# Kernel optimization log

Hardware: AMD Instinct MI355X
Metric: run time of the kernel (lower is better)

Reference implementation:

```python
import jax, jax.numpy as jnp
import numpy as np

N = 50000
E = 400000
C_IN = 32
H = 64
RATIO = 0.5
SEQ_LEN = 5


def setup_inputs() -> dict:
    key = jax.random.key(0)
    ks = jax.random.split(key, 12)
    x = jax.random.normal(ks[0], (N, C_IN), jnp.float32)
    row = jax.random.randint(ks[1], (E,), 0, N, jnp.int32)
    off = jax.random.randint(ks[2], (E,), 1, N, jnp.int32)
    col = ((row + off) % N).astype(jnp.int32)  # no self-loops
    edge_index = jnp.stack([row, col])
    mask = jax.random.uniform(ks[3], (N,)) < 0.5

    def g(k, shape, fan):
        return jax.random.normal(k, shape, jnp.float32) / np.float32(np.sqrt(fan))

    return {
        "x": x, "edge_index": edge_index, "mask": mask,
        "conv0_w": g(ks[4], (C_IN, H), C_IN), "conv0_b": jnp.zeros((H,), jnp.float32),
        "conv1_w": g(ks[5], (H, H), H), "conv1_b": jnp.zeros((H,), jnp.float32),
        "pool_w": g(ks[6], (H,), H),
        "up_w": g(ks[7], (H, H), H), "up_b": jnp.zeros((H,), jnp.float32),
        "lstm0_w_ih": g(ks[8], (4 * H, H), H), "lstm0_w_hh": g(ks[9], (4 * H, H), H),
        "lstm0_b_ih": jnp.zeros((4 * H,), jnp.float32), "lstm0_b_hh": jnp.zeros((4 * H,), jnp.float32),
        "fin_w_ih": g(ks[10], (4 * H, H), H), "fin_w_hh": g(ks[11], (4 * H, H), H),
        "fin_b_ih": jnp.zeros((4 * H,), jnp.float32), "fin_b_hh": jnp.zeros((4 * H,), jnp.float32),
    }


def _coalesce(row, col, w, n):
    # sum duplicate (row, col) entries; output sorted by (row, col)
    key = row.astype(np.int64) * n + col.astype(np.int64)
    uk, inv = np.unique(key, return_inverse=True)
    w2 = np.bincount(inv, weights=w.astype(np.float64), minlength=uk.shape[0]).astype(np.float32)
    return uk // n, uk % n, w2


def _augment_adj(row, col, w, n):
    # remove self loops, add self loops (weight 1), compute A @ A (sparse), remove self loops
    m = row != col
    row = np.concatenate([row[m].astype(np.int64), np.arange(n, dtype=np.int64)])
    col = np.concatenate([col[m].astype(np.int64), np.arange(n, dtype=np.int64)])
    w = np.concatenate([w[m].astype(np.float32), np.ones(n, np.float32)])
    row, col, w = _coalesce(row, col, w, n)  # CSR-ordered
    cnt = np.bincount(row, minlength=n)
    indptr = np.concatenate([[0], np.cumsum(cnt)])
    dk = cnt[col]                      # out-degree of middle node k for each edge (i,k)
    starts = indptr[col]
    total = int(dk.sum())
    seg = np.repeat(np.cumsum(dk) - dk, dk)
    gi = np.repeat(starts, dk) + (np.arange(total) - seg)
    oi = np.repeat(row, dk)
    oj = col[gi]
    ow = np.repeat(w, dk) * w[gi]
    r2, c2, w2 = _coalesce(oi, oj, ow, n)
    m2 = r2 != c2
    return r2[m2], c2[m2], w2[m2]


def _gcn(x, row, col, ew, n, W, b):
    # GCNConv(improved=True): self-loop weight 2.0, symmetric deg^-1/2 normalization,
    # aggregate messages at target (col)
    h = x @ W
    loop = jnp.arange(n, dtype=row.dtype)
    r = jnp.concatenate([row, loop])
    c = jnp.concatenate([col, loop])
    w = jnp.concatenate([ew, jnp.full((n,), 2.0, ew.dtype)])
    deg = jax.ops.segment_sum(w, c, num_segments=n)
    dinv = jnp.where(deg > 0, jax.lax.rsqrt(deg), 0.0)
    norm = dinv[r] * w * dinv[c]
    out = jax.ops.segment_sum(norm[:, None] * h[r], c, num_segments=n)
    return out + b


def _sequences(x, mi):
    # sliding window [idx-L+1, idx] per masked node, zero left-padded
    t = mi[:, None] + jnp.arange(SEQ_LEN)[None, :] - (SEQ_LEN - 1)  # [M, L]
    return jnp.where((t >= 0)[:, :, None], x[jnp.clip(t, 0)], 0.0)


def _lstm_last(seq, w_ih, w_hh, b_ih, b_hh):
    # torch LSTM gate order: i, f, g, o; zero init state; return last hidden
    h = jnp.zeros((seq.shape[0], w_hh.shape[1]), seq.dtype)
    c = jnp.zeros_like(h)
    def step(carry, xt):
        h, c = carry
        g = xt @ w_ih.T + h @ w_hh.T + b_ih + b_hh
        i, f, gg, o = jnp.split(g, 4, axis=-1)
        c = jax.nn.sigmoid(f) * c + jax.nn.sigmoid(i) * jnp.tanh(gg)
        h = jax.nn.sigmoid(o) * jnp.tanh(c)
        return (h, c), None
    (h, _), _ = jax.lax.scan(step, (h, c), jnp.swapaxes(seq, 0, 1))
    return h


def reference(x, edge_index, mask, conv0_w, conv0_b, conv1_w, conv1_b, pool_w,
              up_w, up_b, lstm0_w_ih, lstm0_w_hh, lstm0_b_ih, lstm0_b_hh,
              fin_w_ih, fin_w_hh, fin_b_ih, fin_b_hh):
    n = x.shape[0]
    row0, col0 = edge_index[0], edge_index[1]
    ew0 = jnp.ones((row0.shape[0],), x.dtype)

    # down conv 0
    x1 = jax.nn.relu(_gcn(x, row0, col0, ew0, n, conv0_w, conv0_b))

    # augment_adj: sparse (A+I)^2 without diagonal (structural, constant)
    r2, c2, w2 = _augment_adj(np.asarray(row0), np.asarray(col0),
                              np.ones(row0.shape[0], np.float32), n)

    # TopKPooling: score = tanh((x.w)/||w||), keep top ceil(ratio*n)
    score = jnp.tanh((x1 @ pool_w) / jnp.linalg.norm(pool_w))
    k = int(np.ceil(RATIO * n))
    perm = np.argsort(-np.asarray(score), kind="stable")[:k]
    remap = np.full(n, -1, np.int64)
    remap[perm] = np.arange(k)
    keep = (remap[r2] >= 0) & (remap[c2] >= 0)
    pr = jnp.asarray(remap[r2[keep]].astype(np.int32))
    pc = jnp.asarray(remap[c2[keep]].astype(np.int32))
    pw = jnp.asarray(w2[keep])
    permj = jnp.asarray(perm.astype(np.int32))
    xp = x1[permj] * score[permj][:, None]

    # down conv 1 on pooled graph
    x2 = jax.nn.relu(_gcn(xp, pr, pc, pw, k, conv1_w, conv1_b))

    # up path (depth=1): LSTM over skip features at masked nodes
    mi = jnp.asarray(np.where(np.asarray(mask))[0].astype(np.int32))
    h0 = _lstm_last(_sequences(x1, mi), lstm0_w_ih, lstm0_w_hh, lstm0_b_ih, lstm0_b_hh)
    res = x1.at[mi].set(h0)
    up = jnp.zeros_like(x1).at[permj].set(x2)
    xo = _gcn(res + up, row0, col0, ew0, n, up_w, up_b)  # last level: no activation

    # final LSTM on masked nodes
    hf = _lstm_last(_sequences(xo, mi), fin_w_ih, fin_w_hh, fin_b_ih, fin_b_hh)
    return xo.at[mi].set(hf)
```

## Files before the change

kernel.cpp:

```cpp
#include <hip/hip_runtime.h>
#include <math.h>

#define NN 50000
#define EE 400000
#define CINV 32
#define KKEEP 25000
#define SEQL 5
#define HASH_BITS 20
#define HASH_SIZE (1u<<HASH_BITS)
#define HASH_MASK (HASH_SIZE-1u)
#define HEMPTY 0xFFFFFFFFu
#define PSB 196

typedef float vf4 __attribute__((ext_vector_type(4)));

__device__ __forceinline__ float sigm(float x){ return __builtin_amdgcn_rcpf(1.f+__expf(-x)); }
__device__ __forceinline__ float ftanh(float x){ return 1.f - 2.f*__builtin_amdgcn_rcpf(1.f+__expf(2.f*x)); }

__global__ void k_init(uint2* __restrict__ hash, unsigned* __restrict__ hist,
                       int* __restrict__ degcnt, int* __restrict__ diagint,
                       int* __restrict__ fillc, int* __restrict__ minv,
                       unsigned* scal, unsigned long long* selp,
                       const float* __restrict__ w0, const float* __restrict__ b0i,
                       const float* __restrict__ b0h, const float* __restrict__ wf,
                       const float* __restrict__ bfi, const float* __restrict__ bfh,
                       float* __restrict__ WT0, float* __restrict__ WTf,
                       float* __restrict__ bs0, float* __restrict__ bsf){
  int i = blockIdx.x*256 + threadIdx.x;
  if (i < (int)HASH_SIZE) hash[i] = make_uint2(HEMPTY, 0u);
  if (i < 4*65536) hist[i] = 0u;
  if (i < NN){ degcnt[i]=0; diagint[i]=0; fillc[i]=0; minv[i]=-1; }
  if (i < 256*64){
    int r = i>>6, k = i&63;
    int dst = k*256 + (r&63)*4 + (r>>6);
    WT0[dst] = w0[i];
    WTf[dst] = wf[i];
  }
  if (i < 256){
    int dst = (i&63)*4 + (i>>6);
    bs0[dst]=b0i[i]+b0h[i]; bsf[dst]=bfi[i]+bfh[i];
  }
  if (i == 0){ scal[0]=0u; scal[1]=0u; scal[3]=KKEEP; selp[0]=0ull; }
}

__global__ void k_phase2(const int* __restrict__ row, const int* __restrict__ col,
                         const int* __restrict__ mp, int* __restrict__ degcnt,
                         uint2* __restrict__ tab, unsigned* scal,
                         const float* __restrict__ X, const float* __restrict__ W,
                         float* __restrict__ Y){
  int idx = blockIdx.x*256 + threadIdx.x;
  if (idx < EE){
    int c = col[idx];
    atomicAdd(&degcnt[c], 1);
    unsigned key = (unsigned)row[idx]*50000u + (unsigned)c;
    unsigned h = (key*2654435761u) >> (32-HASH_BITS);
    for(;;){
      unsigned old = atomicCAS(&tab[h].x, HEMPTY, key);
      if (old==HEMPTY || old==key){ atomicAdd(&tab[h].y, 1u); break; }
      h = (h+1)&HASH_MASK;
    }
  }
  if (idx < NN/4){ if ((unsigned)mp[idx] > 1u) atomicOr(&scal[1], 1u); }
  if (idx < NN*16){
    int i = idx>>4, fq = idx&15;
    const vf4* X4 = (const vf4*)&X[i*CINV];
    const vf4* W4 = (const vf4*)W;
    vf4 acc = {0.f,0.f,0.f,0.f};
    #pragma unroll
    for (int kq=0;kq<CINV/4;kq++){
      vf4 xv = X4[kq];
      #pragma unroll
      for (int u=0;u<4;u++) acc += xv[u] * W4[(kq*4+u)*16+fq];
    }
    ((vf4*)Y)[i*16+fq] = acc;
  }
}

__global__ void k_psum1(const int* __restrict__ deg, int* __restrict__ part,
                        int* __restrict__ bsum, float* __restrict__ dinv){
  __shared__ int sc[256];
  int b = blockIdx.x, t = threadIdx.x, i = b*256+t;
  int v = (i<NN) ? deg[i] : 0;
  if (i < NN) dinv[i] = rsqrtf((float)v + 2.0f);
  sc[t] = v; __syncthreads();
  for (int o=1;o<256;o<<=1){
    int x = (t>=o) ? sc[t-o] : 0;
    __syncthreads();
    sc[t] += x;
    __syncthreads();
  }
  if (i < NN) part[i] = sc[t]-v;
  if (t == 255) bsum[b] = sc[255];
}
__global__ void k_psum3(const int* __restrict__ part, const int* __restrict__ bsum,
                        int* __restrict__ indptr){
  __shared__ int sc[256];
  int t = threadIdx.x;
  int v = (t<PSB) ? bsum[t] : 0;
  sc[t] = v; __syncthreads();
  for (int o=1;o<256;o<<=1){
    int x = (t>=o) ? sc[t-o] : 0;
    __syncthreads();
    sc[t] += x;
    __syncthreads();
  }
  int bb = blockIdx.x;
  int ex = sc[bb] - ((bb<PSB) ? bsum[bb] : 0);
  int i = bb*256 + t;
  if (i < NN) indptr[i] = part[i] + ex;
  if (i == 0) indptr[NN] = EE;
}

__global__ void k_phase4(const int* __restrict__ row, const int* __restrict__ col,
                         const int* __restrict__ indptr, int* __restrict__ fillc,
                         int* __restrict__ csr_r, const uint2* __restrict__ tab,
                         int* __restrict__ diagint, const void* __restrict__ mp,
                         unsigned* scal, int* __restrict__ mlist, int* __restrict__ minv){
  int idx = blockIdx.x*256 + threadIdx.x;
  if (idx < EE){
    int r = row[idx], c = col[idx];
    int pos = indptr[c] + atomicAdd(&fillc[c], 1);
    csr_r[pos] = r;
    unsigned rkey = (unsigned)c*50000u + (unsigned)r;
    unsigned h = (rkey*2654435761u) >> (32-HASH_BITS);
    for(;;){
      unsigned kk = tab[h].x;
      if (kk==rkey){ atomicAdd(&diagint[r], (int)tab[h].y); break; }
      if (kk==HEMPTY) break;
      h = (h+1)&HASH_MASK;
    }
  } else {
    int i = idx - EE;
    if (i < NN){
      int mv = scal[1] ? (int)((const unsigned char*)mp)[i] : ((const int*)mp)[i];
      if (mv){ int p = (int)atomicAdd(&scal[0], 1u); mlist[p] = i; minv[i] = p; }
    }
  }
}

__global__ void k_mm64v(const float* __restrict__ X, const float* __restrict__ W, float* __restrict__ Y){
  int idx = blockIdx.x*256 + threadIdx.x;
  if (idx >= NN*16) return;
  int i = idx>>4, fq = idx&15;
  const vf4* X4 = (const vf4*)&X[i*64];
  const vf4* W4 = (const vf4*)W;
  vf4 acc = {0.f,0.f,0.f,0.f};
  #pragma unroll
  for (int kq=0;kq<16;kq++){
    vf4 xv = X4[kq];
    #pragma unroll
    for (int u=0;u<4;u++) acc += xv[u] * W4[(kq*4+u)*16+fq];
  }
  ((vf4*)Y)[i*16+fq] = acc;
}

__global__ void g_gcn0(const int* __restrict__ indptr, const int* __restrict__ csr_r,
                       const float* __restrict__ dinv, const float* __restrict__ H,
                       const float* __restrict__ b, const float* __restrict__ pw,
                       float* __restrict__ out, unsigned long long* __restrict__ keys,
                       float* __restrict__ score, unsigned* __restrict__ hist){
  int node = blockIdx.x*4 + (threadIdx.x>>6), lane = threadIdx.x&63;
  if (node >= NN) return;
  int s = __builtin_amdgcn_readfirstlane(indptr[node]);
  int e = __builtin_amdgcn_readfirstlane(indptr[node+1]);
  int deg = e - s;
  float a0=0.f,a1=0.f,a2=0.f,a3=0.f;
  for (int base=0; base<deg; base+=64){
    int take = min(64, deg-base);
    bool act = lane < take;
    int ii = act ? csr_r[s+base+lane] : 0;
    float dv = act ? dinv[ii] : 0.f;
    int j=0;
    for (; j+4<=take; j+=4){
      int r0=__shfl(ii,j,64), r1=__shfl(ii,j+1,64), r2=__shfl(ii,j+2,64), r3=__shfl(ii,j+3,64);
      float d0=__shfl(dv,j,64), d1=__shfl(dv,j+1,64), d2=__shfl(dv,j+2,64), d3=__shfl(dv,j+3,64);
      a0 += d0*H[(size_t)r0*64+lane];
      a1 += d1*H[(size_t)r1*64+lane];
      a2 += d2*H[(size_t)r2*64+lane];
      a3 += d3*H[(size_t)r3*64+lane];
    }
    for (; j<take; j++){
      int r0=__shfl(ii,j,64); float d0=__shfl(dv,j,64);
      a0 += d0*H[(size_t)r0*64+lane];
    }
  }
  float acc = (a0+a1)+(a2+a3);
  float di = dinv[node];
  float v = di*acc + 2.f*di*di*H[(size_t)node*64+lane] + b[lane];
  float x1v = fmaxf(v, 0.f);
  out[(size_t)node*64+lane] = x1v;
  float pv = pw[lane];
  float nq = pv*pv;
  float dq = x1v*pv;
  for (int o=32;o;o>>=1){ nq += __shfl_down(nq, o, 64); dq += __shfl_down(dq, o, 64); }
  if (lane==0){
    float sv = tanhf(dq / sqrtf(nq));
    sv = sv + 0.0f;
    score[node] = sv;
    unsigned u = __float_as_uint(sv);
    unsigned asc = (u>>31) ? ~u : (u | 0x80000000u);
    unsigned desc = ~asc;
    keys[node] = (((unsigned long long)desc)<<32) | (unsigned)node;
    atomicAdd(&hist[desc>>16], 1u);
  }
}
__global__ void g_t2(const int* __restrict__ indptr, const int* __restrict__ csr_r,
                     const float* __restrict__ dinv1, const float* __restrict__ hp,
                     float* __restrict__ t2){
  int node = blockIdx.x*4 + (threadIdx.x>>6), lane = threadIdx.x&63;
  if (node >= NN) return;
  int s = __builtin_amdgcn_readfirstlane(indptr[node]);
  int e = __builtin_amdgcn_readfirstlane(indptr[node+1]);
  int deg = e - s;
  float a0 = dinv1[node]*hp[(size_t)node*64+lane];
  float a1 = 0.f;
  for (int base=0; base<deg; base+=64){
    int take = min(64, deg-base);
    bool act = lane < take;
    int ii = act ? csr_r[s+base+lane] : 0;
    float dv = act ? dinv1[ii] : 0.f;
    int j=0;
    for (; j+2<=take; j+=2){
      float d0=__shfl(dv,j,64), d1=__shfl(dv,j+1,64);
      int r0=__shfl(ii,j,64), r1=__shfl(ii,j+1,64);
      if (d0!=0.f) a0 += d0*hp[(size_t)r0*64+lane];
      if (d1!=0.f) a1 += d1*hp[(size_t)r1*64+lane];
    }
    for (; j<take; j++){
      float d0=__shfl(dv,j,64); int r0=__shfl(ii,j,64);
      if (d0!=0.f) a0 += d0*hp[(size_t)r0*64+lane];
    }
  }
  t2[(size_t)node*64+lane] = a0+a1;
}
__global__ void g_agg2y(const int* __restrict__ indptr, const int* __restrict__ csr_r,
                        const float* __restrict__ t2, const float* __restrict__ hp,
                        const float* __restrict__ dinv1, const int* __restrict__ diagint,
                        const int* __restrict__ kp, const float* __restrict__ b1,
                        const float* __restrict__ C, const float* __restrict__ Hbuf,
                        const int* __restrict__ minv, float* __restrict__ D){
  int node = blockIdx.x*4 + (threadIdx.x>>6), lane = threadIdx.x&63;
  if (node >= NN) return;
  int mv = minv[node];
  float base = (mv >= 0) ? Hbuf[(size_t)mv*64+lane] : C[(size_t)node*64+lane];
  float add = 0.f;
  if (kp[node]){
    int s = __builtin_amdgcn_readfirstlane(indptr[node]);
    int e = __builtin_amdgcn_readfirstlane(indptr[node+1]);
    int deg = e - s;
    float a0 = t2[(size_t)node*64+lane];
    float a1=0.f,a2=0.f,a3=0.f;
    for (int bs2=0; bs2<deg; bs2+=64){
      int take = min(64, deg-bs2);
      bool act = lane < take;
      int ii = act ? csr_r[s+bs2+lane] : 0;
      int j=0;
      for (; j+4<=take; j+=4){
        int r0=__shfl(ii,j,64), r1=__shfl(ii,j+1,64), r2=__shfl(ii,j+2,64), r3=__shfl(ii,j+3,64);
        a0 += t2[(size_t)r0*64+lane];
        a1 += t2[(size_t)r1*64+lane];
        a2 += t2[(size_t)r2*64+lane];
        a3 += t2[(size_t)r3*64+lane];
      }
      for (; j<take; j++){
        int r0=__shfl(ii,j,64);
        a0 += t2[(size_t)r0*64+lane];
      }
    }
    float acc = (a0+a1)+(a2+a3);
    float di = dinv1[node], hv = hp[(size_t)node*64+lane];
    float diag = (float)(diagint[node] + 1);
    float v = di*(acc - diag*di*hv) + 2.f*di*di*hv + b1[lane];
    add = fmaxf(v, 0.f);
  }
  D[(size_t)node*64+lane] = base + add;
}
__global__ void g_up(const int* __restrict__ indptr, const int* __restrict__ csr_r,
                     const float* __restrict__ dinv, const float* __restrict__ H,
                     const float* __restrict__ b, float* __restrict__ xo, float* __restrict__ out){
  int node = blockIdx.x*4 + (threadIdx.x>>6), lane = threadIdx.x&63;
  if (node >= NN) return;
  int s = __builtin_amdgcn_readfirstlane(indptr[node]);
  int e = __builtin_amdgcn_readfirstlane(indptr[node+1]);
  int deg = e - s;
  float a0=0.f,a1=0.f,a2=0.f,a3=0.f;
  for (int base=0; base<deg; base+=64){
    int take = min(64, deg-base);
    bool act = lane < take;
    int ii = act ? csr_r[s+base+lane] : 0;
    float dv = act ? dinv[ii] : 0.f;
    int j=0;
    for (; j+4<=take; j+=4){
      int r0=__shfl(ii,j,64), r1=__shfl(ii,j+1,64), r2=__shfl(ii,j+2,64), r3=__shfl(ii,j+3,64);
      float d0=__shfl(dv,j,64), d1=__shfl(dv,j+1,64), d2=__shfl(dv,j+2,64), d3=__shfl(dv,j+3,64);
      a0 += d0*H[(size_t)r0*64+lane];
      a1 += d1*H[(size_t)r1*64+lane];
      a2 += d2*H[(size_t)r2*64+lane];
      a3 += d3*H[(size_t)r3*64+lane];
    }
    for (; j<take; j++){
      int r0=__shfl(ii,j,64); float d0=__shfl(dv,j,64);
      a0 += d0*H[(size_t)r0*64+lane];
    }
  }
  float acc = (a0+a1)+(a2+a3);
  float di = dinv[node];
  float v = di*acc + 2.f*di*di*H[(size_t)node*64+lane] + b[lane];
  xo[(size_t)node*64+lane] = v; out[(size_t)node*64+lane] = v;
}

__global__ void k_hist(const unsigned long long* __restrict__ keys, unsigned* __restrict__ hist,
                       const unsigned long long* __restrict__ selp, int round){
  int i = blockIdx.x*256 + threadIdx.x;
  if (i >= NN) return;
  unsigned long long key = keys[i];
  int shift = 48 - 16*round;
  if ((key>>(shift+16)) == selp[0])
    atomicAdd(&hist[(unsigned)((key>>shift)&0xFFFFull)], 1u);
}
__global__ void k_pick(const unsigned* __restrict__ hist, unsigned long long* selp, unsigned* scal){
  __shared__ unsigned csum[256];
  __shared__ unsigned bins[256];
  __shared__ int schunk;
  int t = threadIdx.x;
  const uint4* h4 = (const uint4*)(hist + t*256);
  unsigned s = 0;
  #pragma unroll 8
  for (int j=0;j<64;j++){ uint4 v = h4[j]; s += v.x+v.y+v.z+v.w; }
  csum[t] = s;
  __syncthreads();
  if (t==0){
    unsigned rem = scal[3];
    int chunk = 255;
    for (int c2=0;c2<256;c2++){ unsigned cc=csum[c2]; if (rem>cc) rem-=cc; else { chunk=c2; break; } }
    schunk = chunk; scal[3] = rem;
  }
  __syncthreads();
  bins[t] = hist[schunk*256 + t];
  __syncthreads();
  if (t==0){
    unsigned rem = scal[3];
    int bin = schunk*256 + 255;
    for (int b=0;b<256;b++){ unsigned hv=bins[b]; if (rem>hv) rem-=hv; else { bin = schunk*256 + b; break; } }
    selp[0] = (selp[0]<<16) | (unsigned long long)(unsigned)bin;
    scal[3] = rem;
  }
}
__global__ void k_tsg(const int* __restrict__ indptr, const int* __restrict__ csr_r,
                      const unsigned long long* __restrict__ keys,
                      const unsigned long long* __restrict__ selp,
                      int* __restrict__ kp, int* __restrict__ ts){
  int i = blockIdx.x*256 + threadIdx.x;
  if (i >= NN) return;
  unsigned long long sp = selp[0];
  int s = indptr[i], e = indptr[i+1];
  int self = (keys[i] <= sp) ? 1 : 0;
  kp[i] = self;
  int acc = self;
  for (int j=s;j<e;j++) acc += (keys[csr_r[j]] <= sp) ? 1 : 0;
  ts[i] = acc;
}
__global__ void k_csgmm(const int* __restrict__ indptr, const int* __restrict__ csr_r,
                        const int* __restrict__ ts, const int* __restrict__ diagint,
                        const int* __restrict__ kp, float* __restrict__ dinv1,
                        const float* __restrict__ X, const float* __restrict__ W,
                        const float* __restrict__ sc, float* __restrict__ Y){
  int idx = blockIdx.x*256 + threadIdx.x;
  if (idx < NN*16){
    int i = idx>>4, fq = idx&15;
    if (!kp[i]) return;
    const vf4* X4 = (const vf4*)&X[i*64];
    const vf4* W4 = (const vf4*)W;
    vf4 acc = {0.f,0.f,0.f,0.f};
    #pragma unroll
    for (int kq=0;kq<16;kq++){
      vf4 xv = X4[kq];
      #pragma unroll
      for (int u=0;u<4;u++) acc += xv[u] * W4[(kq*4+u)*16+fq];
    }
    acc *= sc[i];
    ((vf4*)Y)[i*16+fq] = acc;
  } else {
    int i = idx - NN*16;
    if (i >= NN) return;
    int s = indptr[i], e = indptr[i+1];
    int acc = ts[i];
    for (int j=s;j<e;j++) acc += ts[csr_r[j]];
    dinv1[i] = kp[i] ? rsqrtf((float)(acc - diagint[i] - 1) + 2.0f) : 0.f;
  }
}

__global__ __launch_bounds__(256) void k_xw(const float* __restrict__ src,
        const float* __restrict__ WT, const float* __restrict__ bsum,
        float* __restrict__ XW){
  __shared__ vf4 Wl[4096];
  int t = threadIdx.x;
  const vf4* Wg = (const vf4*)WT;
  for (int u=t; u<4096; u+=256) Wl[u] = Wg[u];
  int fq = t & 63, wv = t >> 6;
  vf4 bias = ((const vf4*)bsum)[fq];
  __syncthreads();
  for (int g = blockIdx.x*4 + wv; g < NN/4; g += gridDim.x*4){
    int n0 = g*4;
    const vf4* X4 = (const vf4*)&src[(size_t)n0*64];
    vf4 a0=bias, a1=bias, a2=bias, a3=bias;
    #pragma unroll 4
    for (int kq=0;kq<16;kq++){
      vf4 x0 = X4[kq], x1 = X4[16+kq], x2 = X4[32+kq], x3 = X4[48+kq];
      vf4 w0 = Wl[(kq*4+0)*64+fq];
      vf4 w1 = Wl[(kq*4+1)*64+fq];
      vf4 w2 = Wl[(kq*4+2)*64+fq];
      vf4 w3 = Wl[(kq*4+3)*64+fq];
      a0 += x0.x*w0 + x0.y*w1 + x0.z*w2 + x0.w*w3;
      a1 += x1.x*w0 + x1.y*w1 + x1.z*w2 + x1.w*w3;
      a2 += x2.x*w0 + x2.y*w1 + x2.z*w2 + x2.w*w3;
      a3 += x3.x*w0 + x3.y*w1 + x3.z*w2 + x3.w*w3;
    }
    vf4* Y = (vf4*)XW;
    Y[(size_t)n0*64 + fq]       = a0;
    Y[(size_t)n0*64 + 64 + fq]  = a1;
    Y[(size_t)n0*64 + 128 + fq] = a2;
    Y[(size_t)n0*64 + 192 + fq] = a3;
  }
}

__global__ __launch_bounds__(256) void k_rec(const float* __restrict__ XW,
        const float* __restrict__ whh, const float* __restrict__ bsum,
        const int* __restrict__ mlist, const unsigned* __restrict__ scal,
        float* __restrict__ dst, int scatter){
  int M = (int)scal[0];
  if (M < 0 || M > NN) M = 0;
  int task = blockIdx.x;
  if (task*4 >= M) return;
  int w = threadIdx.x>>6, lane = threadIdx.x&63;
  int r = w*64 + lane;
  const vf4* g4 = (const vf4*)&whh[(size_t)r*64];
  vf4 wh[16];
  #pragma unroll
  for (int j=0;j<16;j++) wh[j] = g4[j];
  __shared__ float sh[4][64];
  __shared__ float gates[4][4][64];
  int m = task*4 + w;
  bool valid = (m < M);
  int node = mlist[valid ? m : (M-1)];
  node = min(max(node, 0), NN-1);
  const vf4* XW4 = (const vf4*)XW;
  vf4 bp = ((const vf4*)bsum)[lane];
  vf4 xs0, xs1, xs2, xs3, xs4;
  {
    int r0 = node - 4, r1 = node - 3;
    xs0 = (r0 >= 0) ? XW4[(size_t)r0*64 + lane] : bp;
    xs1 = (r1 >= 0) ? XW4[(size_t)r1*64 + lane] : bp;
  }
  float c, h;
  {
    c = sigm(xs0.x)*ftanh(xs0.z);
    h = sigm(xs0.w)*ftanh(c);
    sh[w][lane] = h;
  }
  __syncthreads();
  #pragma unroll
  for (int t=1;t<SEQL;t++){
    if (t==1){ int ri = node-2; xs2 = (ri>=0) ? XW4[(size_t)ri*64+lane] : bp; }
    if (t==2){ int ri = node-1; xs3 = (ri>=0) ? XW4[(size_t)ri*64+lane] : bp; }
    if (t==3){ xs4 = XW4[(size_t)node*64 + lane]; }
    vf4 a0={0,0,0,0}, a1={0,0,0,0}, a2={0,0,0,0}, a3={0,0,0,0};
    #pragma unroll
    for (int j=0;j<16;j++){
      vf4 wj = wh[j];
      a0 += (*(const vf4*)&sh[0][j*4]) * wj;
      a1 += (*(const vf4*)&sh[1][j*4]) * wj;
      a2 += (*(const vf4*)&sh[2][j*4]) * wj;
      a3 += (*(const vf4*)&sh[3][j*4]) * wj;
    }
    gates[0][w][lane] = a0.x+a0.y+a0.z+a0.w;
    gates[1][w][lane] = a1.x+a1.y+a1.z+a1.w;
    gates[2][w][lane] = a2.x+a2.y+a2.z+a2.w;
    gates[3][w][lane] = a3.x+a3.y+a3.z+a3.w;
    __syncthreads();
    vf4 xv = (t==1) ? xs1 : (t==2) ? xs2 : (t==3) ? xs3 : xs4;
    float gi = gates[w][0][lane] + xv.x;
    float gf = gates[w][1][lane] + xv.y;
    float gg = gates[w][2][lane] + xv.z;
    float go = gates[w][3][lane] + xv.w;
    c = sigm(gf)*c + sigm(gi)*ftanh(gg);
    h = sigm(go)*ftanh(c);
    sh[w][lane] = h;
    __syncthreads();
  }
  if (valid){
    size_t o = scatter ? ((size_t)node*64 + lane) : ((size_t)m*64 + lane);
    dst[o] = h;
  }
}

extern "C" void kernel_launch(void* const* d_in, const int* in_sizes, int n_in,
                              void* d_out, int out_size, void* d_ws, size_t ws_size,
                              hipStream_t stream) {
  const float* x   = (const float*)d_in[0];
  const int*   ei  = (const int*)d_in[1];
  const int*   row = ei;
  const int*   col = ei + EE;
  const void*  mp  = d_in[2];
  const float* W0  = (const float*)d_in[3];
  const float* b0  = (const float*)d_in[4];
  const float* W1  = (const float*)d_in[5];
  const float* b1  = (const float*)d_in[6];
  const float* pw  = (const float*)d_in[7];
  const float* Wu  = (const float*)d_in[8];
  const float* bu  = (const float*)d_in[9];
  const float* l0wih=(const float*)d_in[10];
  const float* l0whh=(const float*)d_in[11];
  const float* l0bih=(const float*)d_in[12];
  const float* l0bhh=(const float*)d_in[13];
  const float* lfwih=(const float*)d_in[14];
  const float* lfwhh=(const float*)d_in[15];
  const float* lfbih=(const float*)d_in[16];
  const float* lfbhh=(const float*)d_in[17];

  char* wp = (char*)d_ws;
  auto alloc = [&](size_t bytes)->char*{ char* p = wp; wp += ((bytes+255)/256)*256; return p; };
  float* A     = (float*)alloc((size_t)NN*64*4);
  float* B     = (float*)alloc((size_t)NN*64*4);
  float* C     = (float*)alloc((size_t)NN*64*4);
  float* D     = (float*)alloc((size_t)NN*64*4);
  float* Ebuf  = (float*)alloc((size_t)NN*64*4);
  float* Hbuf  = (float*)alloc((size_t)NN*64*4);
  float* XW    = (float*)alloc((size_t)NN*256*4);
  float* WT0   = (float*)alloc((size_t)256*64*4);
  float* WTf   = (float*)alloc((size_t)256*64*4);
  float* bs0   = (float*)alloc((size_t)256*4);
  float* bsf   = (float*)alloc((size_t)256*4);
  float* score = (float*)alloc((size_t)NN*4);
  float* dinv0 = (float*)alloc((size_t)NN*4);
  float* dinv1 = (float*)alloc((size_t)NN*4);
  unsigned long long* keys = (unsigned long long*)alloc((size_t)NN*8);
  int* degcnt  = (int*)alloc((size_t)NN*4);
  int* diagint = (int*)alloc((size_t)NN*4);
  int* ts      = (int*)alloc((size_t)NN*4);
  int* kp      = (int*)alloc((size_t)NN*4);
  int* mlist   = (int*)alloc((size_t)NN*4);
  int* minv    = (int*)alloc((size_t)NN*4);
  int* indptr  = (int*)alloc((size_t)(NN+1)*4);
  int* part    = (int*)alloc((size_t)NN*4);
  int* fillc   = (int*)alloc((size_t)NN*4);
  int* bsum    = (int*)alloc((size_t)256*4);
  int* csr_r   = (int*)alloc((size_t)EE*4);
  uint2* hash  = (uint2*)alloc((size_t)HASH_SIZE*8);
  unsigned* hist=(unsigned*)alloc((size_t)4*65536*4);
  unsigned* scal=(unsigned*)alloc(256);
  unsigned long long* selp = (unsigned long long*)(scal + 4);

  #define GRID1(n) dim3(((n)+255)/256), dim3(256), 0, stream
  #define GRIDW dim3((NN+3)/4), dim3(256), 0, stream

  k_init<<<GRID1(HASH_SIZE)>>>(hash, hist, degcnt, diagint, fillc, minv,
                               scal, selp, l0wih, l0bih, l0bhh, lfwih, lfbih, lfbhh,
                               WT0, WTf, bs0, bsf);
  k_phase2<<<GRID1(NN*16)>>>(row, col, (const int*)mp, degcnt, hash, scal, x, W0, A);
  k_psum1<<<dim3(PSB),dim3(256),0,stream>>>(degcnt, part, bsum, dinv0);
  k_psum3<<<dim3(PSB),dim3(256),0,stream>>>(part, bsum, indptr);
  k_phase4<<<GRID1(EE+NN)>>>(row, col, indptr, fillc, csr_r, hash, diagint, mp, scal, mlist, minv);

  g_gcn0<<<GRIDW>>>(indptr, csr_r, dinv0, A, b0, pw, C, keys, score, hist);

  k_pick<<<dim3(1),dim3(256),0,stream>>>(hist, selp, scal);
  for (int r2=1;r2<4;r2++){
    k_hist<<<GRID1(NN)>>>(keys, hist + r2*65536, selp, r2);
    k_pick<<<dim3(1),dim3(256),0,stream>>>(hist + r2*65536, selp, scal);
  }
  k_tsg<<<GRID1(NN)>>>(indptr, csr_r, keys, selp, kp, ts);
  k_csgmm<<<GRID1(NN*16+NN)>>>(indptr, csr_r, ts, diagint, kp, dinv1, C, W1, score, Ebuf);
  g_t2<<<GRIDW>>>(indptr, csr_r, dinv1, Ebuf, A);

  k_xw<<<dim3(512),dim3(256),0,stream>>>(C, WT0, bs0, XW);
  k_rec<<<dim3(12500),dim3(256),0,stream>>>(XW, l0whh, bs0, mlist, scal, Hbuf, 0);

  g_agg2y<<<GRIDW>>>(indptr, csr_r, A, Ebuf, dinv1, diagint, kp, b1, C, Hbuf, minv, D);

  k_mm64v<<<GRID1(NN*16)>>>(D, Wu, Ebuf);
  g_up<<<GRIDW>>>(indptr, csr_r, dinv0, Ebuf, bu, B, (float*)d_out);

  k_xw<<<dim3(512),dim3(256),0,stream>>>(B, WTf, bsf, XW);
  k_rec<<<dim3(12500),dim3(256),0,stream>>>(XW, lfwhh, bsf, mlist, scal, (float*)d_out, 1);
  #undef GRIDW
  #undef GRID1
}
```

Before: 648.5 us.

## Fuse top-k radix select, LSTM input matmul, t2 aggregation and up-projection kernels

Replaces the 7 launches of the 16-bit radix select (k_pick/k_hist) with a single-block 8-bit refinement running in block 0 of a new k_sel kernel. The other blocks of k_sel compute the LSTM input projection for C at the same time. The t2 aggregation and the first LSTM recurrence are merged into one launch by interleaving block roles. The 64x64 up-projection matmul is folded into the agg2 kernel through shared memory, which removes the D buffer. The aim is to cut launch overhead and serialization. The cost is that the selection now runs on one block with six serial passes over all keys.

```diff
diff --git a/kernel.cpp b/kernel.cpp
--- a/kernel.cpp
+++ b/kernel.cpp
@@ -24,11 +24,12 @@
                        const float* __restrict__ w0, const float* __restrict__ b0i,
                        const float* __restrict__ b0h, const float* __restrict__ wf,
                        const float* __restrict__ bfi, const float* __restrict__ bfh,
+                       const float* __restrict__ wu, float* __restrict__ WuT,
                        float* __restrict__ WT0, float* __restrict__ WTf,
                        float* __restrict__ bs0, float* __restrict__ bsf){
   int i = blockIdx.x*256 + threadIdx.x;
   if (i < (int)HASH_SIZE) hash[i] = make_uint2(HEMPTY, 0u);
-  if (i < 4*65536) hist[i] = 0u;
+  if (i < 65536) hist[i] = 0u;
   if (i < NN){ degcnt[i]=0; diagint[i]=0; fillc[i]=0; minv[i]=-1; }
   if (i < 256*64){
     int r = i>>6, k = i&63;
@@ -36,6 +37,7 @@
     WT0[dst] = w0[i];
     WTf[dst] = wf[i];
   }
+  if (i < 64*64) WuT[i] = wu[((i&63)<<6) | (i>>6)];
   if (i < 256){
     int dst = (i&63)*4 + (i>>6);
     bs0[dst]=b0i[i]+b0h[i]; bsf[dst]=bfi[i]+bfh[i];
@@ -136,22 +138,6 @@
       if (mv){ int p = (int)atomicAdd(&scal[0], 1u); mlist[p] = i; minv[i] = p; }
     }
   }
-}
-
-__global__ void k_mm64v(const float* __restrict__ X, const float* __restrict__ W, float* __restrict__ Y){
-  int idx = blockIdx.x*256 + threadIdx.x;
-  if (idx >= NN*16) return;
-  int i = idx>>4, fq = idx&15;
-  const vf4* X4 = (const vf4*)&X[i*64];
-  const vf4* W4 = (const vf4*)W;
-  vf4 acc = {0.f,0.f,0.f,0.f};
-  #pragma unroll
-  for (int kq=0;kq<16;kq++){
-    vf4 xv = X4[kq];
-    #pragma unroll
-    for (int u=0;u<4;u++) acc += xv[u] * W4[(kq*4+u)*16+fq];
-  }
-  ((vf4*)Y)[i*16+fq] = acc;
 }
 
 __global__ void g_gcn0(const int* __restrict__ indptr, const int* __restrict__ csr_r,
@@ -204,43 +190,244 @@
     atomicAdd(&hist[desc>>16], 1u);
   }
 }
-__global__ void g_t2(const int* __restrict__ indptr, const int* __restrict__ csr_r,
-                     const float* __restrict__ dinv1, const float* __restrict__ hp,
-                     float* __restrict__ t2){
-  int node = blockIdx.x*4 + (threadIdx.x>>6), lane = threadIdx.x&63;
-  if (node >= NN) return;
-  int s = __builtin_amdgcn_readfirstlane(indptr[node]);
-  int e = __builtin_amdgcn_readfirstlane(indptr[node+1]);
-  int deg = e - s;
-  float a0 = dinv1[node]*hp[(size_t)node*64+lane];
-  float a1 = 0.f;
-  for (int base=0; base<deg; base+=64){
-    int take = min(64, deg-base);
-    bool act = lane < take;
-    int ii = act ? csr_r[s+base+lane] : 0;
-    float dv = act ? dinv1[ii] : 0.f;
-    int j=0;
-    for (; j+2<=take; j+=2){
-      float d0=__shfl(dv,j,64), d1=__shfl(dv,j+1,64);
-      int r0=__shfl(ii,j,64), r1=__shfl(ii,j+1,64);
-      if (d0!=0.f) a0 += d0*hp[(size_t)r0*64+lane];
-      if (d1!=0.f) a1 += d1*hp[(size_t)r1*64+lane];
-    }
-    for (; j<take; j++){
-      float d0=__shfl(dv,j,64); int r0=__shfl(ii,j,64);
-      if (d0!=0.f) a0 += d0*hp[(size_t)r0*64+lane];
-    }
-  }
-  t2[(size_t)node*64+lane] = a0+a1;
-}
-__global__ void g_agg2y(const int* __restrict__ indptr, const int* __restrict__ csr_r,
-                        const float* __restrict__ t2, const float* __restrict__ hp,
+
+__global__ __launch_bounds__(256) void k_sel(const unsigned* __restrict__ hist,
+        const unsigned long long* __restrict__ keys, unsigned long long* __restrict__ selp,
+        const float* __restrict__ src, const float* __restrict__ WT,
+        const float* __restrict__ bsum, float* __restrict__ XW){
+  __shared__ vf4 Wl[4096];
+  int t = threadIdx.x;
+  if (blockIdx.x == 0){
+    unsigned* csum = (unsigned*)&Wl[0];
+    unsigned* bins = (unsigned*)&Wl[64];
+    __shared__ int schunk;
+    __shared__ unsigned srem;
+    __shared__ unsigned long long spfx;
+    const uint4* h4 = (const uint4*)(hist + t*256);
+    unsigned s = 0;
+    #pragma unroll 8
+    for (int j=0;j<64;j++){ uint4 v = h4[j]; s += v.x+v.y+v.z+v.w; }
+    csum[t] = s;
+    __syncthreads();
+    if (t==0){
+      unsigned rem = KKEEP;
+      int chunk = 255;
+      for (int c2=0;c2<256;c2++){ unsigned cc=csum[c2]; if (rem>cc) rem-=cc; else { chunk=c2; break; } }
+      schunk = chunk; srem = rem;
+    }
+    __syncthreads();
+    bins[t] = hist[schunk*256 + t];
+    __syncthreads();
+    if (t==0){
+      unsigned rem = srem;
+      int bin = schunk*256 + 255;
+      for (int b=0;b<256;b++){ unsigned hv=bins[b]; if (rem>hv) rem-=hv; else { bin = schunk*256 + b; break; } }
+      spfx = (unsigned long long)(unsigned)bin;
+      srem = rem;
+    }
+    __syncthreads();
+    for (int rd=0; rd<6; rd++){
+      int shift = 40 - 8*rd;
+      bins[t] = 0u;
+      __syncthreads();
+      unsigned long long pfx = spfx;
+      for (int i=t; i<NN; i+=256){
+        unsigned long long key = keys[i];
+        if ((key >> (shift+8)) == pfx)
+          atomicAdd(&bins[(unsigned)((key>>shift)&0xFFull)], 1u);
+      }
+      __syncthreads();
+      if (t==0){
+        unsigned rem = srem;
+        int bin = 255;
+        for (int b=0;b<256;b++){ unsigned hv=bins[b]; if (rem>hv) rem-=hv; else { bin=b; break; } }
+        spfx = (spfx<<8) | (unsigned long long)(unsigned)bin;
+        srem = rem;
+      }
+      __syncthreads();
+    }
+    if (t==0) selp[0] = spfx;
+  } else {
+    const vf4* Wg = (const vf4*)WT;
+    for (int u=t; u<4096; u+=256) Wl[u] = Wg[u];
+    int fq = t & 63, wv = t >> 6;
+    vf4 bias = ((const vf4*)bsum)[fq];
+    __syncthreads();
+    for (int g = (blockIdx.x-1)*4 + wv; g < NN/4; g += 512*4){
+      int n0 = g*4;
+      const vf4* X4 = (const vf4*)&src[(size_t)n0*64];
+      vf4 a0=bias, a1=bias, a2=bias, a3=bias;
+      #pragma unroll 4
+      for (int kq=0;kq<16;kq++){
+        vf4 x0 = X4[kq], x1 = X4[16+kq], x2 = X4[32+kq], x3 = X4[48+kq];
+        vf4 w0 = Wl[(kq*4+0)*64+fq];
+        vf4 w1 = Wl[(kq*4+1)*64+fq];
+        vf4 w2 = Wl[(kq*4+2)*64+fq];
+        vf4 w3 = Wl[(kq*4+3)*64+fq];
+        a0 += x0.x*w0 + x0.y*w1 + x0.z*w2 + x0.w*w3;
+        a1 += x1.x*w0 + x1.y*w1 + x1.z*w2 + x1.w*w3;
+        a2 += x2.x*w0 + x2.y*w1 + x2.z*w2 + x2.w*w3;
+        a3 += x3.x*w0 + x3.y*w1 + x3.z*w2 + x3.w*w3;
+      }
+      vf4* Y = (vf4*)XW;
+      Y[(size_t)n0*64 + fq]       = a0;
+      Y[(size_t)n0*64 + 64 + fq]  = a1;
+      Y[(size_t)n0*64 + 128 + fq] = a2;
+      Y[(size_t)n0*64 + 192 + fq] = a3;
+    }
+  }
+}
+
+__global__ void k_tsg(const int* __restrict__ indptr, const int* __restrict__ csr_r,
+                      const unsigned long long* __restrict__ keys,
+                      const unsigned long long* __restrict__ selp,
+                      int* __restrict__ kp, int* __restrict__ ts){
+  int i = blockIdx.x*256 + threadIdx.x;
+  if (i >= NN) return;
+  unsigned long long sp = selp[0];
+  int s = indptr[i], e = indptr[i+1];
+  int self = (keys[i] <= sp) ? 1 : 0;
+  kp[i] = self;
+  int acc = self;
+  for (int j=s;j<e;j++) acc += (keys[csr_r[j]] <= sp) ? 1 : 0;
+  ts[i] = acc;
+}
+__global__ void k_csgmm(const int* __restrict__ indptr, const int* __restrict__ csr_r,
+                        const int* __restrict__ ts, const int* __restrict__ diagint,
+                        const int* __restrict__ kp, float* __restrict__ dinv1,
+                        const float* __restrict__ X, const float* __restrict__ W,
+                        const float* __restrict__ sc, float* __restrict__ Y){
+  int idx = blockIdx.x*256 + threadIdx.x;
+  if (idx < NN*16){
+    int i = idx>>4, fq = idx&15;
+    if (!kp[i]) return;
+    const vf4* X4 = (const vf4*)&X[i*64];
+    const vf4* W4 = (const vf4*)W;
+    vf4 acc = {0.f,0.f,0.f,0.f};
+    #pragma unroll
+    for (int kq=0;kq<16;kq++){
+      vf4 xv = X4[kq];
+      #pragma unroll
+      for (int u=0;u<4;u++) acc += xv[u] * W4[(kq*4+u)*16+fq];
+    }
+    acc *= sc[i];
+    ((vf4*)Y)[i*16+fq] = acc;
+  } else {
+    int i = idx - NN*16;
+    if (i >= NN) return;
+    int s = indptr[i], e = indptr[i+1];
+    int acc = ts[i];
+    for (int j=s;j<e;j++) acc += ts[csr_r[j]];
+    dinv1[i] = kp[i] ? rsqrtf((float)(acc - diagint[i] - 1) + 2.0f) : 0.f;
+  }
+}
+
+__global__ __launch_bounds__(256) void g_t2rec(
+        const int* __restrict__ indptr, const int* __restrict__ csr_r,
+        const float* __restrict__ dinv1, const float* __restrict__ hp,
+        float* __restrict__ t2,
+        const float* __restrict__ XW, const float* __restrict__ whh,
+        const float* __restrict__ bsum, const int* __restrict__ mlist,
+        const unsigned* __restrict__ scal, float* __restrict__ dst){
+  __shared__ float sh[4][64];
+  __shared__ float gates[4][4][64];
+  int lane = threadIdx.x&63;
+  if (!(blockIdx.x & 1)){
+    int node = (blockIdx.x>>1)*4 + (threadIdx.x>>6);
+    if (node >= NN) return;
+    int s = __builtin_amdgcn_readfirstlane(indptr[node]);
+    int e = __builtin_amdgcn_readfirstlane(indptr[node+1]);
+    int deg = e - s;
+    float a0 = dinv1[node]*hp[(size_t)node*64+lane];
+    float a1 = 0.f;
+    for (int base=0; base<deg; base+=64){
+      int take = min(64, deg-base);
+      bool act = lane < take;
+      int ii = act ? csr_r[s+base+lane] : 0;
+      float dv = act ? dinv1[ii] : 0.f;
+      int j=0;
+      for (; j+2<=take; j+=2){
+        float d0=__shfl(dv,j,64), d1=__shfl(dv,j+1,64);
+        int r0=__shfl(ii,j,64), r1=__shfl(ii,j+1,64);
+        if (d0!=0.f) a0 += d0*hp[(size_t)r0*64+lane];
+        if (d1!=0.f) a1 += d1*hp[(size_t)r1*64+lane];
+      }
+      for (; j<take; j++){
+        float d0=__shfl(dv,j,64); int r0=__shfl(ii,j,64);
+        if (d0!=0.f) a0 += d0*hp[(size_t)r0*64+lane];
+      }
+    }
+    t2[(size_t)node*64+lane] = a0+a1;
+  } else {
+    int M = (int)scal[0];
+    if (M < 0 || M > NN) M = 0;
+    int task = blockIdx.x>>1;
+    if (task*4 >= M) return;
+    int w = threadIdx.x>>6;
+    int r = w*64 + lane;
+    const vf4* g4 = (const vf4*)&whh[(size_t)r*64];
+    vf4 wh[16];
+    #pragma unroll
+    for (int j=0;j<16;j++) wh[j] = g4[j];
+    int m = task*4 + w;
+    bool valid = (m < M);
+    int node = mlist[valid ? m : (M-1)];
+    node = min(max(node, 0), NN-1);
+    const vf4* XW4 = (const vf4*)XW;
+    vf4 bp = ((const vf4*)bsum)[lane];
+    vf4 xs0, xs1, xs2, xs3, xs4;
+    {
+      int r0 = node - 4, r1 = node - 3;
+      xs0 = (r0 >= 0) ? XW4[(size_t)r0*64 + lane] : bp;
+      xs1 = (r1 >= 0) ? XW4[(size_t)r1*64 + lane] : bp;
+    }
+    float c, h;
+    c = sigm(xs0.x)*ftanh(xs0.z);
+    h = sigm(xs0.w)*ftanh(c);
+    sh[w][lane] = h;
+    __syncthreads();
+    #pragma unroll
+    for (int t=1;t<SEQL;t++){
+      if (t==1){ int ri = node-2; xs2 = (ri>=0) ? XW4[(size_t)ri*64+lane] : bp; }
+      if (t==2){ int ri = node-1; xs3 = (ri>=0) ? XW4[(size_t)ri*64+lane] : bp; }
+      if (t==3){ xs4 = XW4[(size_t)node*64 + lane]; }
+      vf4 a0={0,0,0,0}, a1={0,0,0,0}, a2={0,0,0,0}, a3={0,0,0,0};
+      #pragma unroll
+      for (int j=0;j<16;j++){
+        vf4 wj = wh[j];
+        a0 += (*(const vf4*)&sh[0][j*4]) * wj;
+        a1 += (*(const vf4*)&sh[1][j*4]) * wj;
+        a2 += (*(const vf4*)&sh[2][j*4]) * wj;
+        a3 += (*(const vf4*)&sh[3][j*4]) * wj;
+      }
+      gates[0][w][lane] = a0.x+a0.y+a0.z+a0.w;
+      gates[1][w][lane] = a1.x+a1.y+a1.z+a1.w;
+      gates[2][w][lane] = a2.x+a2.y+a2.z+a2.w;
+      gates[3][w][lane] = a3.x+a3.y+a3.z+a3.w;
+      __syncthreads();
+      vf4 xv = (t==1) ? xs1 : (t==2) ? xs2 : (t==3) ? xs3 : xs4;
+      float gi = gates[w][0][lane] + xv.x;
+      float gf = gates[w][1][lane] + xv.y;
+      float gg = gates[w][2][lane] + xv.z;
+      float go = gates[w][3][lane] + xv.w;
+      c = sigm(gf)*c + sigm(gi)*ftanh(gg);
+      h = sigm(go)*ftanh(c);
+      sh[w][lane] = h;
+      __syncthreads();
+    }
+    if (valid) dst[(size_t)m*64 + lane] = h;
+  }
+}
+
+__global__ void g_agg2m(const int* __restrict__ indptr, const int* __restrict__ csr_r,
+                        const float* __restrict__ t2, float* __restrict__ hp,
                         const float* __restrict__ dinv1, const int* __restrict__ diagint,
                         const int* __restrict__ kp, const float* __restrict__ b1,
                         const float* __restrict__ C, const float* __restrict__ Hbuf,
-                        const int* __restrict__ minv, float* __restrict__ D){
-  int node = blockIdx.x*4 + (threadIdx.x>>6), lane = threadIdx.x&63;
-  if (node >= NN) return;
+                        const int* __restrict__ minv, const float* __restrict__ WuT){
+  __shared__ __align__(16) float shD[4][64];
+  int wv = threadIdx.x>>6, lane = threadIdx.x&63;
+  int node = blockIdx.x*4 + wv;
   int mv = minv[node];
   float base = (mv >= 0) ? Hbuf[(size_t)mv*64+lane] : C[(size_t)node*64+lane];
   float add = 0.f;
@@ -273,8 +460,20 @@
     float v = di*(acc - diag*di*hv) + 2.f*di*di*hv + b1[lane];
     add = fmaxf(v, 0.f);
   }
-  D[(size_t)node*64+lane] = base + add;
-}
+  float dval = base + add;
+  shD[wv][lane] = dval;
+  asm volatile("s_waitcnt lgkmcnt(0)" ::: "memory");
+  __builtin_amdgcn_sched_barrier(0);
+  const vf4* Wt4 = (const vf4*)&WuT[(size_t)lane*64];
+  vf4 acc4 = {0.f,0.f,0.f,0.f};
+  #pragma unroll
+  for (int kq=0; kq<16; kq++){
+    vf4 dv = *(const vf4*)&shD[wv][kq*4];
+    acc4 += dv * Wt4[kq];
+  }
+  hp[(size_t)node*64+lane] = acc4.x+acc4.y+acc4.z+acc4.w;
+}
+
 __global__ void g_up(const int* __restrict__ indptr, const int* __restrict__ csr_r,
                      const float* __restrict__ dinv, const float* __restrict__ H,
                      const float* __restrict__ b, float* __restrict__ xo, float* __restrict__ out){
@@ -307,87 +506,6 @@
   float di = dinv[node];
   float v = di*acc + 2.f*di*di*H[(size_t)node*64+lane] + b[lane];
   xo[(size_t)node*64+lane] = v; out[(size_t)node*64+lane] = v;
-}
-
-__global__ void k_hist(const unsigned long long* __restrict__ keys, unsigned* __restrict__ hist,
-                       const unsigned long long* __restrict__ selp, int round){
-  int i = blockIdx.x*256 + threadIdx.x;
-  if (i >= NN) return;
-  unsigned long long key = keys[i];
-  int shift = 48 - 16*round;
-  if ((key>>(shift+16)) == selp[0])
-    atomicAdd(&hist[(unsigned)((key>>shift)&0xFFFFull)], 1u);
-}
-__global__ void k_pick(const unsigned* __restrict__ hist, unsigned long long* selp, unsigned* scal){
-  __shared__ unsigned csum[256];
-  __shared__ unsigned bins[256];
-  __shared__ int schunk;
-  int t = threadIdx.x;
-  const uint4* h4 = (const uint4*)(hist + t*256);
-  unsigned s = 0;
-  #pragma unroll 8
-  for (int j=0;j<64;j++){ uint4 v = h4[j]; s += v.x+v.y+v.z+v.w; }
-  csum[t] = s;
-  __syncthreads();
-  if (t==0){
-    unsigned rem = scal[3];
-    int chunk = 255;
-    for (int c2=0;c2<256;c2++){ unsigned cc=csum[c2]; if (rem>cc) rem-=cc; else { chunk=c2; break; } }
-    schunk = chunk; scal[3] = rem;
-  }
-  __syncthreads();
-  bins[t] = hist[schunk*256 + t];
-  __syncthreads();
-  if (t==0){
-    unsigned rem = scal[3];
-    int bin = schunk*256 + 255;
-    for (int b=0;b<256;b++){ unsigned hv=bins[b]; if (rem>hv) rem-=hv; else { bin = schunk*256 + b; break; } }
-    selp[0] = (selp[0]<<16) | (unsigned long long)(unsigned)bin;
-    scal[3] = rem;
-  }
-}
-__global__ void k_tsg(const int* __restrict__ indptr, const int* __restrict__ csr_r,
-                      const unsigned long long* __restrict__ keys,
-                      const unsigned long long* __restrict__ selp,
-                      int* __restrict__ kp, int* __restrict__ ts){
-  int i = blockIdx.x*256 + threadIdx.x;
-  if (i >= NN) return;
-  unsigned long long sp = selp[0];
-  int s = indptr[i], e = indptr[i+1];
-  int self = (keys[i] <= sp) ? 1 : 0;
-  kp[i] = self;
-  int acc = self;
-  for (int j=s;j<e;j++) acc += (keys[csr_r[j]] <= sp) ? 1 : 0;
-  ts[i] = acc;
-}
-__global__ void k_csgmm(const int* __restrict__ indptr, const int* __restrict__ csr_r,
-                        const int* __restrict__ ts, const int* __restrict__ diagint,
-                        const int* __restrict__ kp, float* __restrict__ dinv1,
-                        const float* __restrict__ X, const float* __restrict__ W,
-                        const float* __restrict__ sc, float* __restrict__ Y){
-  int idx = blockIdx.x*256 + threadIdx.x;
-  if (idx < NN*16){
-    int i = idx>>4, fq = idx&15;
-    if (!kp[i]) return;
-    const vf4* X4 = (const vf4*)&X[i*64];
-    const vf4* W4 = (const vf4*)W;
-    vf4 acc = {0.f,0.f,0.f,0.f};
-    #pragma unroll
-    for (int kq=0;kq<16;kq++){
-      vf4 xv = X4[kq];
-      #pragma unroll
-      for (int u=0;u<4;u++) acc += xv[u] * W4[(kq*4+u)*16+fq];
-    }
-    acc *= sc[i];
-    ((vf4*)Y)[i*16+fq] = acc;
-  } else {
-    int i = idx - NN*16;
-    if (i >= NN) return;
-    int s = indptr[i], e = indptr[i+1];
-    int acc = ts[i];
-    for (int j=s;j<e;j++) acc += ts[csr_r[j]];
-    dinv1[i] = kp[i] ? rsqrtf((float)(acc - diagint[i] - 1) + 2.0f) : 0.f;
-  }
 }
 
 __global__ __launch_bounds__(256) void k_xw(const float* __restrict__ src,
@@ -453,11 +571,9 @@
     xs1 = (r1 >= 0) ? XW4[(size_t)r1*64 + lane] : bp;
   }
   float c, h;
-  {
-    c = sigm(xs0.x)*ftanh(xs0.z);
-    h = sigm(xs0.w)*ftanh(c);
-    sh[w][lane] = h;
-  }
+  c = sigm(xs0.x)*ftanh(xs0.z);
+  h = sigm(xs0.w)*ftanh(c);
+  sh[w][lane] = h;
   __syncthreads();
   #pragma unroll
   for (int t=1;t<SEQL;t++){
@@ -523,12 +639,12 @@
   float* A     = (float*)alloc((size_t)NN*64*4);
   float* B     = (float*)alloc((size_t)NN*64*4);
   float* C     = (float*)alloc((size_t)NN*64*4);
-  float* D     = (float*)alloc((size_t)NN*64*4);
   float* Ebuf  = (float*)alloc((size_t)NN*64*4);
   float* Hbuf  = (float*)alloc((size_t)NN*64*4);
   float* XW    = (float*)alloc((size_t)NN*256*4);
   float* WT0   = (float*)alloc((size_t)256*64*4);
   float* WTf   = (float*)alloc((size_t)256*64*4);
+  float* WuT   = (float*)alloc((size_t)64*64*4);
   float* bs0   = (float*)alloc((size_t)256*4);
   float* bsf   = (float*)alloc((size_t)256*4);
   float* score = (float*)alloc((size_t)NN*4);
@@ -547,7 +663,7 @@
   int* bsum    = (int*)alloc((size_t)256*4);
   int* csr_r   = (int*)alloc((size_t)EE*4);
   uint2* hash  = (uint2*)alloc((size_t)HASH_SIZE*8);
-  unsigned* hist=(unsigned*)alloc((size_t)4*65536*4);
+  unsigned* hist=(unsigned*)alloc((size_t)65536*4);
   unsigned* scal=(unsigned*)alloc(256);
   unsigned long long* selp = (unsigned long long*)(scal + 4);
 
@@ -556,7 +672,7 @@
 
   k_init<<<GRID1(HASH_SIZE)>>>(hash, hist, degcnt, diagint, fillc, minv,
                                scal, selp, l0wih, l0bih, l0bhh, lfwih, lfbih, lfbhh,
-                               WT0, WTf, bs0, bsf);
+                               Wu, WuT, WT0, WTf, bs0, bsf);
   k_phase2<<<GRID1(NN*16)>>>(row, col, (const int*)mp, degcnt, hash, scal, x, W0, A);
   k_psum1<<<dim3(PSB),dim3(256),0,stream>>>(degcnt, part, bsum, dinv0);
   k_psum3<<<dim3(PSB),dim3(256),0,stream>>>(part, bsum, indptr);
@@ -564,21 +680,16 @@
 
   g_gcn0<<<GRIDW>>>(indptr, csr_r, dinv0, A, b0, pw, C, keys, score, hist);
 
-  k_pick<<<dim3(1),dim3(256),0,stream>>>(hist, selp, scal);
-  for (int r2=1;r2<4;r2++){
-    k_hist<<<GRID1(NN)>>>(keys, hist + r2*65536, selp, r2);
-    k_pick<<<dim3(1),dim3(256),0,stream>>>(hist + r2*65536, selp, scal);
-  }
+  k_sel<<<dim3(513),dim3(256),0,stream>>>(hist, keys, selp, C, WT0, bs0, XW);
+
   k_tsg<<<GRID1(NN)>>>(indptr, csr_r, keys, selp, kp, ts);
   k_csgmm<<<GRID1(NN*16+NN)>>>(indptr, csr_r, ts, diagint, kp, dinv1, C, W1, score, Ebuf);
-  g_t2<<<GRIDW>>>(indptr, csr_r, dinv1, Ebuf, A);
-
-  k_xw<<<dim3(512),dim3(256),0,stream>>>(C, WT0, bs0, XW);
-  k_rec<<<dim3(12500),dim3(256),0,stream>>>(XW, l0whh, bs0, mlist, scal, Hbuf, 0);
-
-  g_agg2y<<<GRIDW>>>(indptr, csr_r, A, Ebuf, dinv1, diagint, kp, b1, C, Hbuf, minv, D);
-
-  k_mm64v<<<GRID1(NN*16)>>>(D, Wu, Ebuf);
+
+  g_t2rec<<<dim3(25000),dim3(256),0,stream>>>(indptr, csr_r, dinv1, Ebuf, A,
+                                              XW, l0whh, bs0, mlist, scal, Hbuf);
+
+  g_agg2m<<<GRIDW>>>(indptr, csr_r, A, Ebuf, dinv1, diagint, kp, b1, C, Hbuf, minv, WuT);
+
   g_up<<<GRIDW>>>(indptr, csr_r, dinv0, Ebuf, bu, B, (float*)d_out);
 
   k_xw<<<dim3(512),dim3(256),0,stream>>>(B, WTf, bsf, XW);
```

Result: slower. 849.2 us (+31.0%).
